# Kernel optimization log

Hardware: AMD Instinct MI355X
Metric: run time of the kernel (lower is better)

Reference implementation:

```python
import jax, jax.numpy as jnp
import numpy as np
from jax import lax

BN_EPS = 1e-3
SLOPE = 0.1
CLUSTER_TEMP = 30.0
K = 16
FEAT = 4096  # 8*8*64


def conv_bn_lrelu(x, w, b, g, beta, m, v):
    # Conv2d stride 2, padding 1 (NCHW / OIHW), then eval-mode BatchNorm, then LeakyReLU.
    y = lax.conv_general_dilated(x, w, window_strides=(2, 2), padding=((1, 1), (1, 1)),
                                 dimension_numbers=("NCHW", "OIHW", "NCHW"))
    y = y + b[None, :, None, None]
    scale = g / jnp.sqrt(v + BN_EPS)
    y = y * scale[None, :, None, None] + (beta - m * scale)[None, :, None, None]
    return jnp.where(y > 0, y, SLOPE * y)


def soft_kmeans(data, mu, num_iter, ct):
    # Row L2-normalize (equivalent to diag(1/||x||) @ data)
    data = data / jnp.linalg.norm(data, axis=1, keepdims=True)
    for _ in range(num_iter):
        dist = data @ mu.T                      # [N, K]
        r = jax.nn.softmax(ct * dist, axis=1)   # [N, K]
        mu = (r.T @ data) / r.sum(axis=0)[:, None]  # [K, F]
    dist = data @ mu.T
    r = jax.nn.softmax(ct * dist, axis=1)
    return mu, r, dist


def setup_inputs() -> dict:
    key = jax.random.key(0)
    ks = jax.random.split(key, 12)
    d = {}
    d["x"] = jax.random.normal(ks[0], (256, 3, 64, 64), dtype=jnp.float32)
    # conv1: 3 -> 128
    d["conv1_w"] = jax.random.normal(ks[1], (128, 3, 3, 3), dtype=jnp.float32) * 0.05
    d["conv1_b"] = jnp.zeros((128,), jnp.float32)
    d["bn1_g"] = jnp.ones((128,), jnp.float32)
    d["bn1_b"] = jnp.zeros((128,), jnp.float32)
    d["bn1_m"] = jax.random.normal(ks[2], (128,), dtype=jnp.float32) * 0.1
    d["bn1_v"] = jax.random.uniform(ks[3], (128,), minval=0.5, maxval=1.5, dtype=jnp.float32)
    # conv2: 128 -> 256
    d["conv2_w"] = jax.random.normal(ks[4], (256, 128, 3, 3), dtype=jnp.float32) * 0.02
    d["conv2_b"] = jnp.zeros((256,), jnp.float32)
    d["bn2_g"] = jnp.ones((256,), jnp.float32)
    d["bn2_b"] = jnp.zeros((256,), jnp.float32)
    d["bn2_m"] = jax.random.normal(ks[5], (256,), dtype=jnp.float32) * 0.1
    d["bn2_v"] = jax.random.uniform(ks[6], (256,), minval=0.5, maxval=1.5, dtype=jnp.float32)
    # conv3: 256 -> 64
    d["conv3_w"] = jax.random.normal(ks[7], (64, 256, 3, 3), dtype=jnp.float32) * 0.02
    d["conv3_b"] = jnp.zeros((64,), jnp.float32)
    d["bn3_g"] = jnp.ones((64,), jnp.float32)
    d["bn3_b"] = jnp.zeros((64,), jnp.float32)
    d["bn3_m"] = jax.random.normal(ks[8], (64,), dtype=jnp.float32) * 0.1
    d["bn3_v"] = jax.random.uniform(ks[9], (64,), minval=0.5, maxval=1.5, dtype=jnp.float32)
    # initial cluster centers, torch.rand(K, F)
    d["mu0"] = jax.random.uniform(ks[10], (K, FEAT), dtype=jnp.float32)
    d["num_iter"] = 10
    return d


def reference(x, conv1_w, conv1_b, bn1_g, bn1_b, bn1_m, bn1_v,
              conv2_w, conv2_b, bn2_g, bn2_b, bn2_m, bn2_v,
              conv3_w, conv3_b, bn3_g, bn3_b, bn3_m, bn3_v,
              mu0, num_iter):
    h = conv_bn_lrelu(x, conv1_w, conv1_b, bn1_g, bn1_b, bn1_m, bn1_v)   # [B,128,32,32]
    h = conv_bn_lrelu(h, conv2_w, conv2_b, bn2_g, bn2_b, bn2_m, bn2_v)   # [B,256,16,16]
    h = conv_bn_lrelu(h, conv3_w, conv3_b, bn3_g, bn3_b, bn3_m, bn3_v)   # [B,64,8,8]
    embeds = h.reshape(-1, FEAT)                                          # [B, 4096]
    mu_init, _, _ = soft_kmeans(embeds, mu0, num_iter, CLUSTER_TEMP)
    _, r, _ = soft_kmeans(embeds, lax.stop_gradient(mu_init), 1, CLUSTER_TEMP)
    return r
```

## Files before the change

kernel.cpp:

```cpp
#include <hip/hip_runtime.h>
#include <stdint.h>
#include <stddef.h>

typedef unsigned short u16;
typedef __attribute__((ext_vector_type(8))) short short8;
typedef __attribute__((ext_vector_type(4))) float f32x4;
typedef __attribute__((ext_vector_type(4))) int int4v;

__device__ __forceinline__ float bf2f(u16 u) {
    unsigned x = ((unsigned)u) << 16;
    return __uint_as_float(x);
}
__device__ __forceinline__ u16 f2bf(float f) {
    unsigned x = __float_as_uint(f);
    unsigned r = (x + 0x7fffu + ((x >> 16) & 1u)) >> 16;
    return (u16)r;
}
__device__ __forceinline__ float ldin(const void* p, size_t i, int isbf) {
    return isbf ? bf2f(((const u16*)p)[i]) : ((const float*)p)[i];
}
__device__ __forceinline__ int detect_bf(const void* v1) {
    const u16* ub = (const u16*)v1;
    int ok = 1;
#pragma unroll
    for (int i = 0; i < 16; i++) {
        float f = bf2f(ub[i]);
        if (!(f >= 0.4f && f <= 1.6f)) ok = 0;
    }
    return ok;
}
__device__ __forceinline__ int sw(int r, int c8) {
    return r * 32 + (((c8) ^ (r & 3)) << 3);
}

struct PrepArgs {
    const void *w1, *w2, *w3;
    u16 *W1p, *W2p, *W3p;
    const void *b1, *g1, *be1, *m1, *v1;
    const void *b2, *g2, *be2, *m2, *v2;
    const void *b3, *g3, *be3, *m3, *v3;
    float *es1, *esh1, *es2, *esh2, *es3, *esh3;
    u16 *zb;
};
__device__ __forceinline__ void packw_body(const void* src, u16* dst, int CI, int Kp,
                                           int total, int blk, int t, int isbf) {
    int p = blk * 256 + t;
    if (p >= total) return;
    int co = p / Kp, k = p - co * Kp;
    int tap = k / CI, ci = k - tap * CI;
    u16 v = 0;
    if (tap < 9) {
        size_t si = (size_t)(co * CI + ci) * 9 + tap;
        v = isbf ? ((const u16*)src)[si] : f2bf(((const float*)src)[si]);
    }
    dst[p] = v;
}
__global__ __launch_bounds__(256) void kprep_all(PrepArgs A) {
    int b = blockIdx.x, t = threadIdx.x;
    int isbf = detect_bf(A.v1);
    if (b < 1152) {
        packw_body(A.w2, A.W2p, 128, 1152, 256 * 1152, b, t, isbf);
    } else if (b < 1728) {
        packw_body(A.w3, A.W3p, 256, 2304, 64 * 2304, b - 1152, t, isbf);
    } else if (b < 1744) {
        packw_body(A.w1, A.W1p, 3, 32, 128 * 32, b - 1728, t, isbf);
    } else {
        if (b == 1745) A.zb[t] = 0;
        int u = (b - 1744) * 256 + t;
        const void *bb, *g, *be, *m, *v;
        float *es, *esh;
        int c;
        if (u < 128)      { c = u;       bb=A.b1; g=A.g1; be=A.be1; m=A.m1; v=A.v1; es=A.es1; esh=A.esh1; }
        else if (u < 384) { c = u - 128; bb=A.b2; g=A.g2; be=A.be2; m=A.m2; v=A.v2; es=A.es2; esh=A.esh2; }
        else if (u < 448) { c = u - 384; bb=A.b3; g=A.g3; be=A.be3; m=A.m3; v=A.v3; es=A.es3; esh=A.esh3; }
        else return;
        float sc = ldin(g, c, isbf) / sqrtf(ldin(v, c, isbf) + 1e-3f);
        float sh = (ldin(bb, c, isbf) - ldin(m, c, isbf)) * sc + ldin(be, c, isbf);
        es[c] = sc;
        esh[c] = sh;
    }
}

__global__ void kfallback(u16* __restrict__ out) {
    int i = blockIdx.x * 256 + threadIdx.x;
    if (i < 4096) out[i] = f2bf(0.0625f);
}

__global__ __launch_bounds__(256) void im2col1(const void* __restrict__ x,
                                               u16* __restrict__ A1,
                                               const void* __restrict__ v1ref) {
    int n = blockIdx.x, t = threadIdx.x;
    int isbf = detect_bf(v1ref);
    __shared__ u16 xs[3 * 64 * 64];
    if (isbf) {
        const u16* xp = (const u16*)x + (size_t)n * 12288;
#pragma unroll
        for (int i = t * 8; i < 12288; i += 2048)
            *(int4v*)&xs[i] = *(const int4v*)&xp[i];
    } else {
        const float* xp = (const float*)x + (size_t)n * 12288;
#pragma unroll
        for (int i = t * 4; i < 12288; i += 1024) {
            float4 v = *(const float4*)&xp[i];
            xs[i] = f2bf(v.x); xs[i + 1] = f2bf(v.y);
            xs[i + 2] = f2bf(v.z); xs[i + 3] = f2bf(v.w);
        }
    }
    __syncthreads();
#pragma unroll
    for (int rr = 0; rr < 4; rr++) {
        int m = rr * 256 + t;
        int ox = m & 31, oy = m >> 5;
        alignas(16) u16 row[32];
#pragma unroll
        for (int k = 0; k < 32; k++) {
            u16 val = 0;
            if (k < 27) {
                int tap = k / 3, ci = k - 3 * tap;
                int ky = tap / 3, kx = tap - 3 * ky;
                int iy = 2 * oy - 1 + ky, ix = 2 * ox - 1 + kx;
                if ((unsigned)iy < 64u && (unsigned)ix < 64u)
                    val = xs[ci * 4096 + iy * 64 + ix];
            }
            row[k] = val;
        }
        int4v* dst = (int4v*)(A1 + ((size_t)n * 1024 + m) * 32);
        const int4v* srcv = (const int4v*)row;
#pragma unroll
        for (int q = 0; q < 4; q++) dst[q] = srcv[q];
    }
}

__global__ __launch_bounds__(256) void gemm_conv1(
    const u16* __restrict__ A1, const u16* __restrict__ W,
    const float* __restrict__ es, const float* __restrict__ esh,
    u16* __restrict__ OutB) {
    alignas(16) __shared__ u16 As[128 * 32];
    alignas(16) __shared__ u16 Bs[128 * 32];
    const int t = threadIdx.x;
    const int m0 = blockIdx.x * 128;
    const int lane = t & 63, w = t >> 6;
    const int wm = w & 1, wn = w >> 1;
    const int rA = t >> 2, c8 = t & 3, koff = c8 * 8;

#pragma unroll
    for (int j = 0; j < 2; j++) {
        int4v va = *(const int4v*)(A1 + (size_t)(m0 + j * 64 + rA) * 32 + koff);
        *(int4v*)&As[sw(j * 64 + rA, c8)] = va;
        int4v vb = *(const int4v*)(W + (size_t)(j * 64 + rA) * 32 + koff);
        *(int4v*)&Bs[sw(j * 64 + rA, c8)] = vb;
    }
    __syncthreads();
    const int qc = lane >> 4, fr = lane & 15;
    short8 af[4], bf[4];
#pragma unroll
    for (int i = 0; i < 4; i++) af[i] = *(const short8*)&As[sw(wm * 64 + i * 16 + fr, qc)];
#pragma unroll
    for (int j = 0; j < 4; j++) bf[j] = *(const short8*)&Bs[sw(wn * 64 + j * 16 + fr, qc)];
    f32x4 acc[4][4];
#pragma unroll
    for (int i = 0; i < 4; i++)
#pragma unroll
        for (int j = 0; j < 4; j++) {
#pragma unroll
            for (int q = 0; q < 4; q++) acc[i][j][q] = 0.f;
            acc[i][j] = __builtin_amdgcn_mfma_f32_16x16x32_bf16(af[i], bf[j], acc[i][j], 0, 0, 0);
        }
    float scv[4], shv[4];
#pragma unroll
    for (int j = 0; j < 4; j++) {
        int c = wn * 64 + j * 16 + fr;
        scv[j] = es[c];
        shv[j] = esh[c];
    }
#pragma unroll
    for (int i = 0; i < 4; i++) {
#pragma unroll
        for (int rg = 0; rg < 4; rg++) {
            int m = m0 + wm * 64 + i * 16 + qc * 4 + rg;
            int ox = m & 31, oy = (m >> 5) & 31, n = m >> 10;
            u16* orow = OutB + ((size_t)(n * 32 + oy) * 32 + ox) * 128 + wn * 64 + fr;
#pragma unroll
            for (int j = 0; j < 4; j++) {
                float v = acc[i][j][rg] * scv[j] + shv[j];
                v = (v > 0.f) ? v : 0.1f * v;
                orow[j * 16] = f2bf(v);
            }
        }
    }
}

__global__ __launch_bounds__(512, 2) void gemm_conv2(
    const u16* __restrict__ h1, const u16* __restrict__ W,
    const float* __restrict__ es, const float* __restrict__ esh,
    u16* __restrict__ OutB, const u16* __restrict__ zb) {
    alignas(16) __shared__ u16 smem[4 * 16384];
    u16* const Ab0 = smem;
    u16* const Ab1 = smem + 16384;
    u16* const Bb0 = smem + 32768;
    u16* const Bb1 = smem + 49152;

    const int t = threadIdx.x;
    const int w = t >> 6, l = t & 63;
    const int img = blockIdx.x;
    const int wm = w >> 2, wn = w & 3;
    const int fr = l & 15, qc = l >> 4;

    int aiy0[4], aix0[4], ac8e[4];
    int brow[4];
#pragma unroll
    for (int i = 0; i < 4; ++i) {
        int gi = w * 256 + i * 64 + l;
        int r = gi >> 3, c8d = gi & 7;
        int c8s = c8d ^ (r & 7);
        int oy = r >> 4, ox = r & 15;
        aiy0[i] = 2 * oy - 1;
        aix0[i] = 2 * ox - 1;
        ac8e[i] = c8s * 8;
        brow[i] = r * 1152 + c8s * 8;
    }
    auto mkA = [&](int i, int ky, int kx) -> const u16* {
        int iy = aiy0[i] + ky, ix = aix0[i] + kx;
        if ((unsigned)iy < 32u && (unsigned)ix < 32u)
            return h1 + (size_t)(((img * 32 + iy) * 32 + ix) * 128 + ac8e[i]);
        return zb;
    };
    auto stage = [&](const u16* src, u16* ldsbase, int i) {
        __builtin_amdgcn_global_load_lds(
            (const __attribute__((address_space(1))) void*)src,
            (__attribute__((address_space(3))) void*)(ldsbase + (w * 4 + i) * 512),
            16, 0, 0);
    };

    f32x4 acc[8][4];
#pragma unroll
    for (int mi = 0; mi < 8; ++mi)
#pragma unroll
        for (int nj = 0; nj < 4; ++nj)
#pragma unroll
            for (int q = 0; q < 4; ++q) acc[mi][nj][q] = 0.0f;

    auto do_tile = [&](const u16* A, const u16* B) {
#pragma unroll
        for (int kk = 0; kk < 2; ++kk) {
            const int c8 = kk * 4 + qc;
            short8 a[8], b[4];
#pragma unroll
            for (int q = 0; q < 8; ++q) {
                int row = wm * 128 + q * 16 + fr;
                a[q] = *(const short8*)(A + row * 64 + ((c8 ^ (row & 7)) << 3));
            }
#pragma unroll
            for (int j = 0; j < 4; ++j) {
                int row = wn * 64 + j * 16 + fr;
                b[j] = *(const short8*)(B + row * 64 + ((c8 ^ (row & 7)) << 3));
            }
            __builtin_amdgcn_s_setprio(1);
#pragma unroll
            for (int q = 0; q < 8; ++q)
#pragma unroll
                for (int j = 0; j < 4; ++j)
                    acc[q][j] = __builtin_amdgcn_mfma_f32_16x16x32_bf16(
                        a[q], b[j], acc[q][j], 0, 0, 0);
            __builtin_amdgcn_s_setprio(0);
        }
    };

    const u16* pcur[4];
#pragma unroll
    for (int i = 0; i < 4; ++i) pcur[i] = mkA(i, 0, 0);
#pragma unroll
    for (int i = 0; i < 4; ++i) {
        stage(pcur[i], Ab0, i);
        stage(W + brow[i], Bb0, i);
    }

    for (int tap = 0; tap < 9; ++tap) {
        __syncthreads();
#pragma unroll
        for (int i = 0; i < 4; ++i) {
            stage(pcur[i] + 64, Ab1, i);
            stage(W + brow[i] + (2 * tap + 1) * 64, Bb1, i);
        }
        do_tile(Ab0, Bb0);
        __syncthreads();
        if (tap < 8) {
            const int tap2 = tap + 1;
            const int ky2 = (tap2 >= 6) ? 2 : (tap2 >= 3) ? 1 : 0;
            const int kx2 = tap2 - 3 * ky2;
#pragma unroll
            for (int i = 0; i < 4; ++i) pcur[i] = mkA(i, ky2, kx2);
#pragma unroll
            for (int i = 0; i < 4; ++i) {
                stage(pcur[i], Ab0, i);
                stage(W + brow[i] + (2 * tap + 2) * 64, Bb0, i);
            }
        }
        do_tile(Ab1, Bb1);
    }

    float scv[4], shv[4];
#pragma unroll
    for (int nj = 0; nj < 4; ++nj) {
        int c = wn * 64 + nj * 16 + fr;
        scv[nj] = es[c];
        shv[nj] = esh[c];
    }
#pragma unroll
    for (int mi = 0; mi < 8; ++mi) {
#pragma unroll
        for (int rg = 0; rg < 4; ++rg) {
            int r = wm * 128 + mi * 16 + qc * 4 + rg;
            u16* orow = OutB + ((size_t)img * 256 + r) * 256 + wn * 64 + fr;
#pragma unroll
            for (int nj = 0; nj < 4; ++nj) {
                float v = acc[mi][nj][rg] * scv[nj] + shv[nj];
                v = (v > 0.f) ? v : 0.1f * v;
                orow[nj * 16] = f2bf(v);
            }
        }
    }
}

__global__ __launch_bounds__(256) void gemm_conv3f(
    const u16* __restrict__ Asrc, const u16* __restrict__ W,
    const float* __restrict__ es3, const float* __restrict__ esh3,
    float* __restrict__ dat, u16* __restrict__ datbf,
    const u16* __restrict__ zb) {
    alignas(16) __shared__ u16 smem[4 * 4096];
    __shared__ float red[4];
    u16* const AbP[2] = {smem, smem + 4096};
    u16* const BbP[2] = {smem + 8192, smem + 12288};

    const int t = threadIdx.x;
    const int w = t >> 6, l = t & 63;
    const int lid = blockIdx.x;
    const int xcd = lid & 7, slot = lid >> 3;
    const int img = xcd * 32 + slot;
    const int wm = w & 1, wn = w >> 1;
    const int fr = l & 15, qc = l >> 4;

    int aiy0[2], aix0[2], ac8e[2];
    int brow[2];
#pragma unroll
    for (int i = 0; i < 2; ++i) {
        int g = w * 128 + i * 64 + l;
        int r = g >> 3, c8d = g & 7;
        int c8s = c8d ^ (r & 7);
        int oy = r >> 3, ox = r & 7;
        aiy0[i] = 2 * oy - 1;
        aix0[i] = 2 * ox - 1;
        ac8e[i] = c8s * 8;
        brow[i] = r * 2304 + c8s * 8;
    }
    auto mkA = [&](int i, int ky, int kx) -> const u16* {
        int iy = aiy0[i] + ky, ix = aix0[i] + kx;
        if ((unsigned)iy < 16u && (unsigned)ix < 16u)
            return Asrc + (size_t)(((img * 16 + iy) * 16 + ix) * 256 + ac8e[i]);
        return zb;
    };
    auto stage = [&](const u16* src, u16* ldsbase, int i) {
        __builtin_amdgcn_global_load_lds(
            (const __attribute__((address_space(1))) void*)src,
            (__attribute__((address_space(3))) void*)(ldsbase + (w * 2 + i) * 512),
            16, 0, 0);
    };

    f32x4 acc[2][2];
#pragma unroll
    for (int i = 0; i < 2; i++)
#pragma unroll
        for (int j = 0; j < 2; j++)
#pragma unroll
            for (int q = 0; q < 4; q++) acc[i][j][q] = 0.0f;

    auto do_tile = [&](const u16* A, const u16* B) {
#pragma unroll
        for (int kk = 0; kk < 2; ++kk) {
            const int c8 = kk * 4 + qc;
            short8 a[2], b[2];
#pragma unroll
            for (int i = 0; i < 2; ++i) {
                int row = wm * 32 + i * 16 + fr;
                a[i] = *(const short8*)(A + row * 64 + ((c8 ^ (row & 7)) << 3));
            }
#pragma unroll
            for (int j = 0; j < 2; ++j) {
                int row = wn * 32 + j * 16 + fr;
                b[j] = *(const short8*)(B + row * 64 + ((c8 ^ (row & 7)) << 3));
            }
            __builtin_amdgcn_s_setprio(1);
#pragma unroll
            for (int i = 0; i < 2; ++i)
#pragma unroll
                for (int j = 0; j < 2; ++j)
                    acc[i][j] = __builtin_amdgcn_mfma_f32_16x16x32_bf16(
                        a[i], b[j], acc[i][j], 0, 0, 0);
            __builtin_amdgcn_s_setprio(0);
        }
    };

    const u16* pcur[2];
#pragma unroll
    for (int i = 0; i < 2; ++i) pcur[i] = mkA(i, 0, 0);
#pragma unroll
    for (int i = 0; i < 2; ++i) {
        stage(pcur[i], AbP[0], i);
        stage(W + brow[i], BbP[0], i);
    }

    int flat = 0;
    for (int tap = 0; tap < 9; ++tap) {
        for (int q4 = 0; q4 < 4; ++q4, ++flat) {
            const int cb = flat & 1;
            __syncthreads();
            int ntap = tap, nq = q4 + 1;
            if (nq == 4) { nq = 0; ntap = tap + 1; }
            if (ntap < 9) {
                if (nq == 0) {
                    const int ky = (ntap >= 6) ? 2 : (ntap >= 3) ? 1 : 0;
                    const int kx = ntap - 3 * ky;
#pragma unroll
                    for (int i = 0; i < 2; ++i) pcur[i] = mkA(i, ky, kx);
                }
#pragma unroll
                for (int i = 0; i < 2; ++i) {
                    stage(pcur[i] + nq * 64, AbP[cb ^ 1], i);
                    stage(W + brow[i] + ntap * 256 + nq * 64, BbP[cb ^ 1], i);
                }
            }
            do_tile(AbP[cb], BbP[cb]);
        }
    }

    float vals[2][2][4];
    float ssq = 0.f;
#pragma unroll
    for (int j = 0; j < 2; j++) {
        int c = wn * 32 + j * 16 + fr;
        float sc = es3[c], sh = esh3[c];
#pragma unroll
        for (int i = 0; i < 2; i++) {
#pragma unroll
            for (int rg = 0; rg < 4; rg++) {
                float v = acc[i][j][rg] * sc + sh;
                v = (v > 0.f) ? v : 0.1f * v;
                vals[i][j][rg] = v;
                ssq += v * v;
            }
        }
    }
#pragma unroll
    for (int off = 32; off > 0; off >>= 1) ssq += __shfl_xor(ssq, off);
    if (l == 0) red[w] = ssq;
    __syncthreads();
    float inv = 1.0f / sqrtf(red[0] + red[1] + red[2] + red[3]);
#pragma unroll
    for (int j = 0; j < 2; j++) {
        int c = wn * 32 + j * 16 + fr;
#pragma unroll
        for (int i = 0; i < 2; i++) {
#pragma unroll
            for (int rg = 0; rg < 4; rg++) {
                int row = wm * 32 + i * 16 + qc * 4 + rg;
                size_t idx = (size_t)img * 4096 + c * 64 + row;
                float v = vals[i][j][rg] * inv;
                dat[idx] = v;
                datbf[idx] = f2bf(v);
            }
        }
    }
}

__global__ __launch_bounds__(256) void kgr(const u16* __restrict__ dbf,
                                           const float* __restrict__ dat,
                                           const void* __restrict__ mu0,
                                           float* __restrict__ Gp,
                                           float* __restrict__ rb0,
                                           const void* __restrict__ v1ref) {
    const int b = blockIdx.x, t = threadIdx.x;
    __shared__ float part[16][4];
    __shared__ float ds[16];

    if (b < 128) {
        const int tile = b & 15, s = b >> 4;
        const int m0 = (tile & 3) * 64, n0 = (tile >> 2) * 64;
        const int lane = t & 63, w = t >> 6;
        const int wm = w & 1, wn = w >> 1;
        const int fr = lane & 15, qc = lane >> 4;

        f32x4 acc[2][2];
#pragma unroll
        for (int i = 0; i < 2; i++)
#pragma unroll
            for (int j = 0; j < 2; j++)
#pragma unroll
                for (int q = 0; q < 4; q++) acc[i][j][q] = 0.0f;

        const u16* a0p = dbf + (size_t)(m0 + wm * 32 + fr) * 4096 + s * 512 + qc * 8;
        const u16* a1p = a0p + 16 * 4096;
        const u16* b0p = dbf + (size_t)(n0 + wn * 32 + fr) * 4096 + s * 512 + qc * 8;
        const u16* b1p = b0p + 16 * 4096;

        short8 Pa0[4], Pa1[4], Pb0[4], Pb1[4];
        short8 Qa0[4], Qa1[4], Qb0[4], Qb1[4];
        auto ldc = [&](short8* A0, short8* A1, short8* B0, short8* B1, int c) {
#pragma unroll
            for (int u = 0; u < 4; ++u) {
                const int o = c * 128 + u * 32;
                A0[u] = *(const short8*)(a0p + o);
                A1[u] = *(const short8*)(a1p + o);
                B0[u] = *(const short8*)(b0p + o);
                B1[u] = *(const short8*)(b1p + o);
            }
        };
        auto mmc = [&](short8* A0, short8* A1, short8* B0, short8* B1) {
#pragma unroll
            for (int u = 0; u < 4; ++u) {
                acc[0][0] = __builtin_amdgcn_mfma_f32_16x16x32_bf16(A0[u], B0[u], acc[0][0], 0, 0, 0);
                acc[0][1] = __builtin_amdgcn_mfma_f32_16x16x32_bf16(A0[u], B1[u], acc[0][1], 0, 0, 0);
                acc[1][0] = __builtin_amdgcn_mfma_f32_16x16x32_bf16(A1[u], B0[u], acc[1][0], 0, 0, 0);
                acc[1][1] = __builtin_amdgcn_mfma_f32_16x16x32_bf16(A1[u], B1[u], acc[1][1], 0, 0, 0);
            }
        };
        ldc(Pa0, Pa1, Pb0, Pb1, 0);
#pragma unroll
        for (int c = 0; c < 2; ++c) {
            ldc(Qa0, Qa1, Qb0, Qb1, 2 * c + 1);
            mmc(Pa0, Pa1, Pb0, Pb1);
            if (c < 1) ldc(Pa0, Pa1, Pb0, Pb1, 2 * c + 2);
            mmc(Qa0, Qa1, Qb0, Qb1);
        }

        float* gp = Gp + (size_t)s * 65536;
#pragma unroll
        for (int j = 0; j < 2; j++) {
            int cc = n0 + wn * 32 + j * 16 + fr;
#pragma unroll
            for (int i = 0; i < 2; i++)
#pragma unroll
                for (int rg = 0; rg < 4; rg++) {
                    int row = m0 + wm * 32 + i * 16 + qc * 4 + rg;
                    gp[row * 256 + cc] = acc[i][j][rg];
                }
        }
    } else {
        const int n = b - 128;
        const int isbf = detect_bf(v1ref);
        const int lane = t & 63, wv = t >> 6;
        float d[16];
#pragma unroll
        for (int j = 0; j < 16; j++) d[j] = dat[(size_t)n * 4096 + j * 256 + t];
#pragma unroll
        for (int k = 0; k < 16; k++) {
            float a = 0.f;
            if (isbf) {
                const u16* mp = (const u16*)mu0 + (size_t)k * 4096;
#pragma unroll
                for (int j = 0; j < 16; j++) a = fmaf(d[j], bf2f(mp[j * 256 + t]), a);
            } else {
                const float* mp = (const float*)mu0 + (size_t)k * 4096;
#pragma unroll
                for (int j = 0; j < 16; j++) a = fmaf(d[j], mp[j * 256 + t], a);
            }
#pragma unroll
            for (int off = 32; off > 0; off >>= 1) a += __shfl_xor(a, off);
            if (lane == 0) part[k][wv] = a;
        }
        __syncthreads();
        if (t < 16) {
            float dk = part[t][0] + part[t][1] + part[t][2] + part[t][3];
            ds[t] = dk;
            __syncthreads();
            float mx = -1e30f;
#pragma unroll
            for (int j = 0; j < 16; j++) mx = fmaxf(mx, ds[j]);
            float sum = 0.f;
#pragma unroll
            for (int j = 0; j < 16; j++) sum += __expf(30.f * (ds[j] - mx));
            rb0[n * 16 + t] = __expf(30.f * (dk - mx)) / sum;
        }
    }
}

__global__ __launch_bounds__(256) void kcomb(const float* __restrict__ Gp,
                                             u16* __restrict__ Ghi,
                                             u16* __restrict__ Glo) {
    const int i = (blockIdx.x * 256 + threadIdx.x) * 4;
    f32x4 s[8];
#pragma unroll
    for (int p = 0; p < 8; p++) s[p] = *(const f32x4*)(Gp + (size_t)p * 65536 + i);
    unsigned long long ph = 0, pl = 0;
#pragma unroll
    for (int q = 0; q < 4; q++) {
        float v = s[0][q];
#pragma unroll
        for (int p = 1; p < 8; p++) v += s[p][q];
        u16 hi = f2bf(v);
        u16 lo = f2bf(v - bf2f(hi));
        ph |= ((unsigned long long)hi) << (16 * q);
        pl |= ((unsigned long long)lo) << (16 * q);
    }
    *(unsigned long long*)(Ghi + i) = ph;
    *(unsigned long long*)(Glo + i) = pl;
}

__global__ __launch_bounds__(512) void kmiter(const u16* __restrict__ Ghi,
                                              const u16* __restrict__ Glo,
                                              const float* __restrict__ rb0,
                                              void* __restrict__ dout,
                                              const void* __restrict__ v1ref) {
    const int t = threadIdx.x;
    const int isbf = detect_bf(v1ref);
    const int lane = t & 63, w = t >> 6;
    const int i0 = w * 32;
    const int col = lane & 15;
    const int q = lane >> 4;

    __shared__ u16 rThi[2][16 * 264];
    __shared__ u16 rTlo[2][16 * 264];
    __shared__ float part[2][8][17];

    short8 gh[2][8], gl[2][8];
#pragma unroll
    for (int sg = 0; sg < 2; sg++) {
        const u16* Ah = Ghi + (size_t)(i0 + sg * 16 + col) * 256 + q * 8;
        const u16* Al = Glo + (size_t)(i0 + sg * 16 + col) * 256 + q * 8;
#pragma unroll
        for (int s = 0; s < 8; s++) {
            gh[sg][s] = *(const short8*)(Ah + s * 32);
            gl[sg][s] = *(const short8*)(Al + s * 32);
        }
    }

    {
        float rv[2][4];
#pragma unroll
        for (int sg = 0; sg < 2; sg++)
#pragma unroll
            for (int rg = 0; rg < 4; rg++) {
                int row = i0 + sg * 16 + q * 4 + rg;
                float v = rb0[row * 16 + col];
                rv[sg][rg] = v;
                u16 hi = f2bf(v);
                rThi[0][col * 264 + row] = hi;
                rTlo[0][col * 264 + row] = f2bf(v - bf2f(hi));
            }
        float s0 = (rv[0][0] + rv[0][1] + rv[0][2] + rv[0][3]) +
                   (rv[1][0] + rv[1][1] + rv[1][2] + rv[1][3]);
        s0 += __shfl_xor(s0, 16);
        s0 += __shfl_xor(s0, 32);
        if (lane < 16) part[0][w][lane] = s0;
    }
    __syncthreads();
    float rsc = 0.f;
#pragma unroll
    for (int ww = 0; ww < 8; ww++) rsc += part[0][ww][col];

    int cur = 0;
    for (int iter = 0; iter < 11; iter++) {
        f32x4 a0[2] = {{0.f, 0.f, 0.f, 0.f}, {0.f, 0.f, 0.f, 0.f}};
        f32x4 a1[2] = {{0.f, 0.f, 0.f, 0.f}, {0.f, 0.f, 0.f, 0.f}};
#pragma unroll
        for (int s = 0; s < 4; s++) {
            short8 bh = *(const short8*)&rThi[cur][col * 264 + s * 32 + q * 8];
            short8 bl = *(const short8*)&rTlo[cur][col * 264 + s * 32 + q * 8];
#pragma unroll
            for (int sg = 0; sg < 2; sg++) {
                a0[sg] = __builtin_amdgcn_mfma_f32_16x16x32_bf16(gh[sg][s], bh, a0[sg], 0, 0, 0);
                a0[sg] = __builtin_amdgcn_mfma_f32_16x16x32_bf16(gl[sg][s], bh, a0[sg], 0, 0, 0);
                a0[sg] = __builtin_amdgcn_mfma_f32_16x16x32_bf16(gh[sg][s], bl, a0[sg], 0, 0, 0);
            }
            short8 bh2 = *(const short8*)&rThi[cur][col * 264 + (s + 4) * 32 + q * 8];
            short8 bl2 = *(const short8*)&rTlo[cur][col * 264 + (s + 4) * 32 + q * 8];
#pragma unroll
            for (int sg = 0; sg < 2; sg++) {
                a1[sg] = __builtin_amdgcn_mfma_f32_16x16x32_bf16(gh[sg][s + 4], bh2, a1[sg], 0, 0, 0);
                a1[sg] = __builtin_amdgcn_mfma_f32_16x16x32_bf16(gl[sg][s + 4], bh2, a1[sg], 0, 0, 0);
                a1[sg] = __builtin_amdgcn_mfma_f32_16x16x32_bf16(gh[sg][s + 4], bl2, a1[sg], 0, 0, 0);
            }
        }
        float nv[2][4];
#pragma unroll
        for (int sg = 0; sg < 2; sg++)
#pragma unroll
            for (int rg = 0; rg < 4; rg++) {
                float dk = (a0[sg][rg] + a1[sg][rg]) / rsc;
                float mx = dk;
#pragma unroll
                for (int o = 1; o < 16; o <<= 1) mx = fmaxf(mx, __shfl_xor(mx, o));
                float e = __expf(30.f * (dk - mx));
                float ssum = e;
#pragma unroll
                for (int o = 1; o < 16; o <<= 1) ssum += __shfl_xor(ssum, o);
                nv[sg][rg] = e / ssum;
            }
        if (iter < 10) {
            const int nxt = cur ^ 1;
#pragma unroll
            for (int sg = 0; sg < 2; sg++)
#pragma unroll
                for (int rg = 0; rg < 4; rg++) {
                    int row = i0 + sg * 16 + q * 4 + rg;
                    u16 hi = f2bf(nv[sg][rg]);
                    rThi[nxt][col * 264 + row] = hi;
                    rTlo[nxt][col * 264 + row] = f2bf(nv[sg][rg] - bf2f(hi));
                }
            float s0 = (nv[0][0] + nv[0][1] + nv[0][2] + nv[0][3]) +
                       (nv[1][0] + nv[1][1] + nv[1][2] + nv[1][3]);
            s0 += __shfl_xor(s0, 16);
            s0 += __shfl_xor(s0, 32);
            if (lane < 16) part[nxt][w][lane] = s0;
            __syncthreads();
            rsc = 0.f;
#pragma unroll
            for (int ww = 0; ww < 8; ww++) rsc += part[nxt][ww][col];
            cur = nxt;
        } else {
#pragma unroll
            for (int sg = 0; sg < 2; sg++)
#pragma unroll
                for (int rg = 0; rg < 4; rg++) {
                    int row = i0 + sg * 16 + q * 4 + rg;
                    if (isbf) ((u16*)dout)[row * 16 + col] = f2bf(nv[sg][rg]);
                    else ((float*)dout)[row * 16 + col] = nv[sg][rg];
                }
        }
    }
}

extern "C" void kernel_launch(void* const* d_in, const int* in_sizes, int n_in,
                              void* d_out, int out_size, void* d_ws, size_t ws_size,
                              hipStream_t stream) {
    const void* x   = d_in[0];
    const void* w1  = d_in[1];
    const void* b1  = d_in[2];
    const void* g1  = d_in[3];
    const void* be1 = d_in[4];
    const void* m1  = d_in[5];
    const void* v1  = d_in[6];
    const void* w2  = d_in[7];
    const void* b2  = d_in[8];
    const void* g2  = d_in[9];
    const void* be2 = d_in[10];
    const void* m2  = d_in[11];
    const void* v2  = d_in[12];
    const void* w3  = d_in[13];
    const void* b3  = d_in[14];
    const void* g3  = d_in[15];
    const void* be3 = d_in[16];
    const void* m3  = d_in[17];
    const void* v3  = d_in[18];
    const void* mu0 = d_in[19];

    char* p = (char*)d_ws;
    size_t used = 0;
    auto alloc = [&](size_t bytes) -> char* {
        char* q = p;
        size_t rb = (bytes + 255) & ~(size_t)255;
        p += rb;
        used += rb;
        return q;
    };
    float* rb0 = (float*)alloc(4096 * 4);
    u16* Ghi = (u16*)alloc((size_t)65536 * 2);
    u16* Glo = (u16*)alloc((size_t)65536 * 2);
    float* Gp = (float*)alloc((size_t)8 * 65536 * 4);
    u16* W1p = (u16*)alloc((size_t)128 * 32 * 2);
    u16* W2p = (u16*)alloc((size_t)256 * 1152 * 2);
    u16* W3p = (u16*)alloc((size_t)64 * 2304 * 2);
    float* es1 = (float*)alloc(128 * 4);
    float* esh1 = (float*)alloc(128 * 4);
    float* es2 = (float*)alloc(256 * 4);
    float* esh2 = (float*)alloc(256 * 4);
    float* es3 = (float*)alloc(64 * 4);
    float* esh3 = (float*)alloc(64 * 4);
    u16* zb = (u16*)alloc(512);
    const size_t R1 = (size_t)256 * 32 * 32 * 128 * 2;
    const size_t R2 = (size_t)256 * 16 * 16 * 256 * 2;
    char* reg1 = alloc(R1);
    char* reg2 = alloc(R2);
    u16* h1 = (u16*)reg1;
    u16* A1 = (u16*)reg2;
    u16* h2 = (u16*)reg2;
    float* dat = (float*)reg1;
    u16* datbf = (u16*)(reg1 + 4194304);

    if (used > ws_size) {
        kfallback<<<16, 256, 0, stream>>>((u16*)d_out);
        return;
    }

    PrepArgs pa = {w1, w2, w3, W1p, W2p, W3p,
                   b1, g1, be1, m1, v1, b2, g2, be2, m2, v2, b3, g3, be3, m3, v3,
                   es1, esh1, es2, esh2, es3, esh3, zb};
    kprep_all<<<1746, 256, 0, stream>>>(pa);
    im2col1<<<256, 256, 0, stream>>>(x, A1, v1);
    gemm_conv1<<<dim3(2048), 256, 0, stream>>>(A1, W1p, es1, esh1, h1);
    gemm_conv2<<<dim3(256), 512, 0, stream>>>(h1, W2p, es2, esh2, h2, zb);
    gemm_conv3f<<<dim3(256), 256, 0, stream>>>(h2, W3p, es3, esh3, dat, datbf, zb);
    kgr<<<dim3(384), 256, 0, stream>>>(datbf, dat, mu0, Gp, rb0, v1);
    kcomb<<<dim3(64), 256, 0, stream>>>(Gp, Ghi, Glo);
    kmiter<<<1, 512, 0, stream>>>(Ghi, Glo, rb0, d_out, v1);
}
```

Measured before the change: 247.0 us.

## Fuse conv1 im2col into the conv1 GEMM kernel

Merges the im2col1 and gemm_conv1 kernels into one per-image kernel that builds im2col tiles in shared memory from the staged input and feeds MFMA directly. This removes the global write and read of the A1 im2col buffer and one launch. The grid shrinks from 2048 to 256 blocks, each looping over 8 sub-tiles with double-buffered LDS, which lowers parallelism and raises shared memory use per block.

```diff
diff --git a/kernel.cpp b/kernel.cpp
--- a/kernel.cpp
+++ b/kernel.cpp
@@ -86,19 +86,28 @@
     if (i < 4096) out[i] = f2bf(0.0625f);
 }
 
-__global__ __launch_bounds__(256) void im2col1(const void* __restrict__ x,
-                                               u16* __restrict__ A1,
-                                               const void* __restrict__ v1ref) {
-    int n = blockIdx.x, t = threadIdx.x;
-    int isbf = detect_bf(v1ref);
+__global__ __launch_bounds__(256) void imc1_gemm(
+    const void* __restrict__ x, const u16* __restrict__ W,
+    const float* __restrict__ es, const float* __restrict__ esh,
+    u16* __restrict__ OutB, const void* __restrict__ v1ref) {
     __shared__ u16 xs[3 * 64 * 64];
+    alignas(16) __shared__ u16 As[2][128 * 32];
+    alignas(16) __shared__ u16 Bs[128 * 32];
+
+    const int img = blockIdx.x, t = threadIdx.x;
+    const int isbf = detect_bf(v1ref);
+    const int lane = t & 63, w = t >> 6;
+    const int wm = w & 1, wn = w >> 1;
+    const int rA = t >> 2, c8 = t & 3, koff = c8 * 8;
+    const int qc = lane >> 4, fr = lane & 15;
+
     if (isbf) {
-        const u16* xp = (const u16*)x + (size_t)n * 12288;
+        const u16* xp = (const u16*)x + (size_t)img * 12288;
 #pragma unroll
         for (int i = t * 8; i < 12288; i += 2048)
             *(int4v*)&xs[i] = *(const int4v*)&xp[i];
     } else {
-        const float* xp = (const float*)x + (size_t)n * 12288;
+        const float* xp = (const float*)x + (size_t)img * 12288;
 #pragma unroll
         for (int i = t * 4; i < 12288; i += 1024) {
             float4 v = *(const float4*)&xp[i];
@@ -106,66 +115,15 @@
             xs[i + 2] = f2bf(v.z); xs[i + 3] = f2bf(v.w);
         }
     }
-    __syncthreads();
-#pragma unroll
-    for (int rr = 0; rr < 4; rr++) {
-        int m = rr * 256 + t;
-        int ox = m & 31, oy = m >> 5;
-        alignas(16) u16 row[32];
-#pragma unroll
-        for (int k = 0; k < 32; k++) {
-            u16 val = 0;
-            if (k < 27) {
-                int tap = k / 3, ci = k - 3 * tap;
-                int ky = tap / 3, kx = tap - 3 * ky;
-                int iy = 2 * oy - 1 + ky, ix = 2 * ox - 1 + kx;
-                if ((unsigned)iy < 64u && (unsigned)ix < 64u)
-                    val = xs[ci * 4096 + iy * 64 + ix];
-            }
-            row[k] = val;
-        }
-        int4v* dst = (int4v*)(A1 + ((size_t)n * 1024 + m) * 32);
-        const int4v* srcv = (const int4v*)row;
-#pragma unroll
-        for (int q = 0; q < 4; q++) dst[q] = srcv[q];
-    }
-}
-
-__global__ __launch_bounds__(256) void gemm_conv1(
-    const u16* __restrict__ A1, const u16* __restrict__ W,
-    const float* __restrict__ es, const float* __restrict__ esh,
-    u16* __restrict__ OutB) {
-    alignas(16) __shared__ u16 As[128 * 32];
-    alignas(16) __shared__ u16 Bs[128 * 32];
-    const int t = threadIdx.x;
-    const int m0 = blockIdx.x * 128;
-    const int lane = t & 63, w = t >> 6;
-    const int wm = w & 1, wn = w >> 1;
-    const int rA = t >> 2, c8 = t & 3, koff = c8 * 8;
-
 #pragma unroll
     for (int j = 0; j < 2; j++) {
-        int4v va = *(const int4v*)(A1 + (size_t)(m0 + j * 64 + rA) * 32 + koff);
-        *(int4v*)&As[sw(j * 64 + rA, c8)] = va;
         int4v vb = *(const int4v*)(W + (size_t)(j * 64 + rA) * 32 + koff);
         *(int4v*)&Bs[sw(j * 64 + rA, c8)] = vb;
     }
     __syncthreads();
-    const int qc = lane >> 4, fr = lane & 15;
-    short8 af[4], bf[4];
-#pragma unroll
-    for (int i = 0; i < 4; i++) af[i] = *(const short8*)&As[sw(wm * 64 + i * 16 + fr, qc)];
+    short8 bf[4];
 #pragma unroll
     for (int j = 0; j < 4; j++) bf[j] = *(const short8*)&Bs[sw(wn * 64 + j * 16 + fr, qc)];
-    f32x4 acc[4][4];
-#pragma unroll
-    for (int i = 0; i < 4; i++)
-#pragma unroll
-        for (int j = 0; j < 4; j++) {
-#pragma unroll
-            for (int q = 0; q < 4; q++) acc[i][j][q] = 0.f;
-            acc[i][j] = __builtin_amdgcn_mfma_f32_16x16x32_bf16(af[i], bf[j], acc[i][j], 0, 0, 0);
-        }
     float scv[4], shv[4];
 #pragma unroll
     for (int j = 0; j < 4; j++) {
@@ -173,18 +131,57 @@
         scv[j] = es[c];
         shv[j] = esh[c];
     }
-#pragma unroll
-    for (int i = 0; i < 4; i++) {
-#pragma unroll
-        for (int rg = 0; rg < 4; rg++) {
-            int m = m0 + wm * 64 + i * 16 + qc * 4 + rg;
-            int ox = m & 31, oy = (m >> 5) & 31, n = m >> 10;
-            u16* orow = OutB + ((size_t)(n * 32 + oy) * 32 + ox) * 128 + wn * 64 + fr;
+
+    for (int sub = 0; sub < 8; ++sub) {
+        const int buf = sub & 1;
+#pragma unroll
+        for (int j = 0; j < 2; j++) {
+            int r = j * 64 + rA;
+            int p = sub * 128 + r;
+            int ox = p & 31, oy = p >> 5;
+            alignas(16) u16 row[8];
+#pragma unroll
+            for (int e = 0; e < 8; e++) {
+                int k = koff + e;
+                u16 val = 0;
+                if (k < 27) {
+                    int tap = k / 3, ci = k - 3 * tap;
+                    int ky = tap / 3, kx = tap - 3 * ky;
+                    int iy = 2 * oy - 1 + ky, ix = 2 * ox - 1 + kx;
+                    if ((unsigned)iy < 64u && (unsigned)ix < 64u)
+                        val = xs[ci * 4096 + iy * 64 + ix];
+                }
+                row[e] = val;
+            }
+            *(int4v*)&As[buf][sw(r, c8)] = *(const int4v*)row;
+        }
+        __syncthreads();
+        short8 af[4];
+#pragma unroll
+        for (int i = 0; i < 4; i++)
+            af[i] = *(const short8*)&As[buf][sw(wm * 64 + i * 16 + fr, qc)];
+        f32x4 acc[4][4];
+#pragma unroll
+        for (int i = 0; i < 4; i++)
 #pragma unroll
             for (int j = 0; j < 4; j++) {
-                float v = acc[i][j][rg] * scv[j] + shv[j];
-                v = (v > 0.f) ? v : 0.1f * v;
-                orow[j * 16] = f2bf(v);
+#pragma unroll
+                for (int q = 0; q < 4; q++) acc[i][j][q] = 0.f;
+                acc[i][j] = __builtin_amdgcn_mfma_f32_16x16x32_bf16(af[i], bf[j], acc[i][j], 0, 0, 0);
+            }
+#pragma unroll
+        for (int i = 0; i < 4; i++) {
+#pragma unroll
+            for (int rg = 0; rg < 4; rg++) {
+                int p = sub * 128 + wm * 64 + i * 16 + qc * 4 + rg;
+                int ox = p & 31, oy = p >> 5;
+                u16* orow = OutB + ((size_t)(img * 32 + oy) * 32 + ox) * 128 + wn * 64 + fr;
+#pragma unroll
+                for (int j = 0; j < 4; j++) {
+                    float v = acc[i][j][rg] * scv[j] + shv[j];
+                    v = (v > 0.f) ? v : 0.1f * v;
+                    orow[j * 16] = f2bf(v);
+                }
             }
         }
     }
@@ -781,7 +778,6 @@
     char* reg1 = alloc(R1);
     char* reg2 = alloc(R2);
     u16* h1 = (u16*)reg1;
-    u16* A1 = (u16*)reg2;
     u16* h2 = (u16*)reg2;
     float* dat = (float*)reg1;
     u16* datbf = (u16*)(reg1 + 4194304);
@@ -795,8 +791,7 @@
                    b1, g1, be1, m1, v1, b2, g2, be2, m2, v2, b3, g3, be3, m3, v3,
                    es1, esh1, es2, esh2, es3, esh3, zb};
     kprep_all<<<1746, 256, 0, stream>>>(pa);
-    im2col1<<<256, 256, 0, stream>>>(x, A1, v1);
-    gemm_conv1<<<dim3(2048), 256, 0, stream>>>(A1, W1p, es1, esh1, h1);
+    imc1_gemm<<<dim3(256), 256, 0, stream>>>(x, W1p, es1, esh1, h1, v1);
     gemm_conv2<<<dim3(256), 512, 0, stream>>>(h1, W2p, es2, esh2, h2, zb);
     gemm_conv3f<<<dim3(256), 256, 0, stream>>>(h2, W3p, es3, esh3, dat, datbf, zb);
     kgr<<<dim3(384), 256, 0, stream>>>(datbf, dat, mu0, Gp, rb0, v1);
```

Result: no change. 246.0 us (-0.4%).
